# Kernel tuning notes

Measured on AMD Instinct MI355X. Metric: run time of the kernel, lower is better.

## Reference

```python
import jax, jax.numpy as jnp
import numpy as np

B, S, E, H = 2, 2048, 1024, 16
D = E // H


def setup_inputs() -> dict:
    key = jax.random.key(0)
    ks = jax.random.split(key, 8)
    hidden_states = jax.random.normal(ks[0], (B, S, E), dtype=jnp.float32)
    # q/k/v projections: small random init
    Wq = jax.random.normal(ks[1], (E, E), dtype=jnp.float32) * 0.02
    Wk = jax.random.normal(ks[2], (E, E), dtype=jnp.float32) * 0.02
    Wv = jax.random.normal(ks[3], (E, E), dtype=jnp.float32) * 0.02
    bq = jnp.zeros((E,), jnp.float32)
    bk = jnp.zeros((E,), jnp.float32)
    bv = jnp.zeros((E,), jnp.float32)
    # hedgehog feature maps: identity init (per init_weights_) + small noise
    eye = jnp.eye(E, dtype=jnp.float32)
    Wfq = eye + jax.random.normal(ks[4], (E, E), dtype=jnp.float32) * 0.02
    Wfk = eye + jax.random.normal(ks[5], (E, E), dtype=jnp.float32) * 0.02
    bfq = jnp.zeros((E,), jnp.float32)
    bfk = jnp.zeros((E,), jnp.float32)
    return dict(hidden_states=hidden_states, Wq=Wq, bq=bq, Wk=Wk, bk=bk,
                Wv=Wv, bv=bv, Wfq=Wfq, bfq=bfq, Wfk=Wfk, bfk=bfk)


def reference(hidden_states, Wq, bq, Wk, bk, Wv, bv, Wfq, bfq, Wfk, bfk):
    b, s, e = hidden_states.shape
    d = e // H
    # feature maps: linear -> linear -> softmax over full hidden dim (before head split)
    q = jax.nn.softmax((hidden_states @ Wq.T + bq) @ Wfq.T + bfq, axis=-1)
    k = jax.nn.softmax((hidden_states @ Wk.T + bk) @ Wfk.T + bfk, axis=-1)
    v = hidden_states @ Wv.T + bv
    split = lambda t: t.reshape(b, s, H, d).transpose(0, 2, 1, 3)  # [B,H,S,D]
    q, k, v = split(q), split(k), split(v)
    scores = jnp.einsum('bhsd,bhtd->bhst', q, k)          # [B,H,S,S], nonnegative
    probs = scores / jnp.sum(scores, axis=-1, keepdims=True)  # sum-normalization
    ctx = jnp.einsum('bhst,bhtd->bhsd', probs, v)
    return ctx.transpose(0, 2, 1, 3).reshape(b, s, e)
```

## Files before the change

### kernel.cpp

```cpp
#include <hip/hip_runtime.h>
#include <math.h>

constexpr int B = 2, S = 2048, E = 1024, H = 16, D = 64;
constexpr int M = B * S;
constexpr int CH = 16;

typedef __attribute__((ext_vector_type(8))) _Float16 half8;
typedef __attribute__((ext_vector_type(4))) float f32x4;
#define MFMA_F16 __builtin_amdgcn_mfma_f32_16x16x32_f16
#define WAITCNT_VM(N) __builtin_amdgcn_s_waitcnt(0xF70 | (N))

__device__ __forceinline__ short f2h(float f) {
  _Float16 h = (_Float16)f;
  short s;
  __builtin_memcpy(&s, &h, 2);
  return s;
}
__device__ __forceinline__ float h2f(short s) {
  _Float16 h;
  __builtin_memcpy(&h, &s, 2);
  return (float)h;
}

__device__ __forceinline__ void gload16(const void* g, const void* l) {
  __builtin_amdgcn_global_load_lds(
      (const __attribute__((address_space(1))) unsigned*)g,
      (__attribute__((address_space(3))) unsigned*)l, 16, 0, 0);
}

struct HArgs {
  const short* A;
  const short* Bm;
  const float* bias;
  short* C;
  float* Zrow;
  int doExp;
};

template <int BM, int WEMIT>
__global__ __launch_bounds__(256, 3) void gemmh(HArgs g0, HArgs g1, HArgs g2, int K, int N) {
  const HArgs h = (blockIdx.z == 0) ? g0 : (blockIdx.z == 1 ? g1 : g2);
  constexpr int SA = BM / 16;
  constexpr int TOT = SA + 8;
  constexpr int PW = TOT / 4;
  constexpr int MT = BM / 32;
  __shared__ short lds[2][TOT * 512];

  const int tid = threadIdx.x, wave = tid >> 6, lane = tid & 63;
  const int bm = blockIdx.x * BM, bn = blockIdx.y * 128;

  const short* gb[PW];
#pragma unroll
  for (int j = 0; j < PW; ++j) {
    const int n = wave * PW + j;
    const short* src; int seg, rowbase;
    if (n < SA) { src = h.A;  seg = n;      rowbase = bm; }
    else        { src = h.Bm; seg = n - SA; rowbase = bn; }
    const int r = seg * 16 + (lane >> 2);
    const int p = lane & 3;
    const int q = (p - ((r >> 1) & 3)) & 3;
    gb[j] = src + (size_t)(rowbase + r) * K + q * 8;
  }

  const int fr = lane & 15, fq = lane >> 4;
  const int wm = (wave & 1) * (BM / 2), wn = (wave >> 1) * 64;
  int ao[MT], bo[4];
#pragma unroll
  for (int mi = 0; mi < MT; ++mi) {
    const int r = wm + mi * 16 + fr;
    ao[mi] = r * 32 + (((fq + ((r >> 1) & 3)) & 3)) * 8;
  }
#pragma unroll
  for (int ni = 0; ni < 4; ++ni) {
    const int r = wn + ni * 16 + fr;
    bo[ni] = BM * 32 + r * 32 + (((fq + ((r >> 1) & 3)) & 3)) * 8;
  }

  f32x4 acc[MT][4] = {};
  const int ldsW = wave * PW * 512;

  auto stageAll = [&](int buf, int k0) {
#pragma unroll
    for (int j = 0; j < PW; ++j)
      gload16(gb[j] + k0, &lds[buf][ldsW + j * 512]);
  };

  stageAll(0, 0);
  stageAll(1, 32);
  int buf = 0;
  for (int k0 = 0; k0 < K; k0 += 32) {
    if (k0 + 32 < K) WAITCNT_VM(PW); else WAITCNT_VM(0);
    __builtin_amdgcn_s_barrier();
    half8 ah[MT], bh4[4];
#pragma unroll
    for (int mi = 0; mi < MT; ++mi) ah[mi] = *(const half8*)&lds[buf][ao[mi]];
#pragma unroll
    for (int ni = 0; ni < 4; ++ni) bh4[ni] = *(const half8*)&lds[buf][bo[ni]];
#pragma unroll
    for (int mi = 0; mi < MT; ++mi)
#pragma unroll
      for (int ni = 0; ni < 4; ++ni)
        acc[mi][ni] = MFMA_F16(ah[mi], bh4[ni], acc[mi][ni], 0, 0, 0);
    __builtin_amdgcn_s_barrier();
    if (k0 + 64 < K) stageAll(buf, k0 + 64);
    buf ^= 1;
  }

  if (WEMIT == 0) {
    short* C = h.C;
    float bv4[4];
#pragma unroll
    for (int ni = 0; ni < 4; ++ni) bv4[ni] = h.bias[bn + wn + ni * 16 + fr];
#pragma unroll
    for (int mi = 0; mi < MT; ++mi)
#pragma unroll
      for (int r2 = 0; r2 < 4; ++r2) {
        const int m = bm + wm + mi * 16 + fq * 4 + r2;
        float vals[4];
#pragma unroll
        for (int ni = 0; ni < 4; ++ni) vals[ni] = acc[mi][ni][r2] + bv4[ni];
        if (h.doExp) {
#pragma unroll
          for (int ni = 0; ni < 4; ++ni) vals[ni] = __expf(vals[ni]);
        }
        if (h.Zrow) {
          float es = vals[0] + vals[1] + vals[2] + vals[3];
#pragma unroll
          for (int off = 1; off < 16; off <<= 1) es += __shfl_xor(es, off, 16);
          if (fr == 0) atomicAdd(&h.Zrow[m], es);
        }
#pragma unroll
        for (int ni = 0; ni < 4; ++ni)
          C[(size_t)m * N + bn + wn + ni * 16 + fr] = f2h(vals[ni]);
      }
  } else {
    short* C = h.C;
#pragma unroll
    for (int ni = 0; ni < 4; ++ni) {
      const int n = bn + wn + ni * 16 + fr;
#pragma unroll
      for (int mi = 0; mi < MT; ++mi) {
        const int m0 = bm + wm + mi * 16 + fq * 4;
#pragma unroll
        for (int r2 = 0; r2 < 4; ++r2)
          C[(size_t)(m0 + r2) * N + n] = f2h(acc[mi][ni][r2]);
      }
    }
  }
}

__global__ __launch_bounds__(256) void prep(
    const float* __restrict__ hs, short* hs_f,
    const float* __restrict__ Wfq, short* Wfq_f,
    const float* __restrict__ Wfk, short* Wfk_f,
    const float* __restrict__ Wv, short* Wv_f,
    const float* __restrict__ Wq, short* WqT_f,
    const float* __restrict__ Wk, short* WkT_f,
    const float* __restrict__ bq, const float* __restrict__ bfq, float* bcQ,
    const float* __restrict__ bk, const float* __restrict__ bfk, float* bcK,
    float* Zk) {
  __shared__ float tb[32][33];
  const int blk = blockIdx.x, tid = threadIdx.x;
  if (blk < 1024) {
#pragma unroll
    for (int p = 0; p < 4; ++p) {
      const int i = blk * 1024 + p * 256 + tid;
      float4 v = ((const float4*)hs)[i];
      ((short4*)hs_f)[i] = make_short4(f2h(v.x), f2h(v.y), f2h(v.z), f2h(v.w));
    }
  } else if (blk < 1792) {
    const int base = blk - 1024;
    const float* src = (base < 256) ? Wfq : (base < 512 ? Wfk : Wv);
    short* dst = (base < 256) ? Wfq_f : (base < 512 ? Wfk_f : Wv_f);
    const int bb = base & 255;
#pragma unroll
    for (int p = 0; p < 4; ++p) {
      const int i = bb * 1024 + p * 256 + tid;
      float4 v = ((const float4*)src)[i];
      ((short4*)dst)[i] = make_short4(f2h(v.x), f2h(v.y), f2h(v.z), f2h(v.w));
    }
  } else if (blk < 3840) {
    const int t = blk - 1792;
    const float* in = (t < 1024) ? Wq : Wk;
    short* oh = (t < 1024) ? WqT_f : WkT_f;
    const int tt = t & 1023;
    const int bx = (tt & 31) * 32, by = (tt >> 5) * 32;
    const int x = tid & 31, y0 = tid >> 5;
#pragma unroll
    for (int i = 0; i < 32; i += 8) tb[y0 + i][x] = in[(size_t)(by + y0 + i) * E + bx + x];
    __syncthreads();
#pragma unroll
    for (int i = 0; i < 32; i += 8)
      oh[(size_t)(bx + y0 + i) * E + by + x] = f2h(tb[x][y0 + i]);
  } else if (blk < 4352) {
    const int t = blk - 3840;
    const float* Wf = (t < 256) ? Wfq : Wfk;
    const float* bin = (t < 256) ? bq : bk;
    const float* bf = (t < 256) ? bfq : bfk;
    float* o = (t < 256) ? bcQ : bcK;
    const int n = (t & 255) * 4 + (tid >> 6);
    const int lane = tid & 63;
    float sacc = 0.f;
    for (int j = lane; j < E; j += 64) sacc += Wf[(size_t)n * E + j] * bin[j];
#pragma unroll
    for (int off = 32; off; off >>= 1) sacc += __shfl_xor(sacc, off, 64);
    if (lane == 0) o[n] = sacc + bf[n];
  } else {
#pragma unroll
    for (int p = 0; p < 4; ++p)
      ((float4*)Zk)[p * 256 + tid] = make_float4(0.f, 0.f, 0.f, 0.f);
  }
}

__global__ __launch_bounds__(256) void kv_part(const short* __restrict__ kh,
                                               const short* __restrict__ vh,
                                               const float* __restrict__ Zk,
                                               float* __restrict__ KVp,
                                               float* __restrict__ ksump) {
  const int bh = blockIdx.x;
  const int b = bh / H, h = bh % H;
  const int t0 = blockIdx.y * 128;
  const short* kbase = kh + (size_t)b * S * E + (size_t)h * D;
  const short* vbase = vh + (size_t)b * S * E + (size_t)h * D;
  __shared__ float ks[16][D];
  __shared__ float vs[16][D];
  __shared__ float invZs[128];
  const int tid = threadIdx.x;
  if (tid < 128) invZs[tid] = 1.0f / Zk[b * S + t0 + tid];
  const int a4 = tid & 15, b4 = tid >> 4;
  const int lt = tid >> 4, d4 = (tid & 15) * 4;
  float acc[4][4] = {};
  float ksm[4] = {};
  for (int ts = 0; ts < 128; ts += 16) {
    __syncthreads();
    const size_t roff = (size_t)(t0 + ts + lt) * E + d4;
    short4 k4 = *(const short4*)(kbase + roff);
    short4 v4 = *(const short4*)(vbase + roff);
    const float iz = invZs[ts + lt];
    ks[lt][d4 + 0] = h2f(k4.x) * iz; ks[lt][d4 + 1] = h2f(k4.y) * iz;
    ks[lt][d4 + 2] = h2f(k4.z) * iz; ks[lt][d4 + 3] = h2f(k4.w) * iz;
    vs[lt][d4 + 0] = h2f(v4.x); vs[lt][d4 + 1] = h2f(v4.y);
    vs[lt][d4 + 2] = h2f(v4.z); vs[lt][d4 + 3] = h2f(v4.w);
    __syncthreads();
#pragma unroll
    for (int tt = 0; tt < 16; ++tt) {
      float kk4[4], vv4[4];
#pragma unroll
      for (int i = 0; i < 4; ++i) kk4[i] = ks[tt][a4 * 4 + i];
#pragma unroll
      for (int j = 0; j < 4; ++j) vv4[j] = vs[tt][b4 * 4 + j];
#pragma unroll
      for (int i = 0; i < 4; ++i) {
        ksm[i] += kk4[i];
#pragma unroll
        for (int j = 0; j < 4; ++j) acc[i][j] = fmaf(kk4[i], vv4[j], acc[i][j]);
      }
    }
  }
  float* kvout = KVp + ((size_t)bh * CH + blockIdx.y) * 4096;
#pragma unroll
  for (int i = 0; i < 4; ++i)
    *(float4*)&kvout[(a4 * 4 + i) * 64 + b4 * 4] =
        make_float4(acc[i][0], acc[i][1], acc[i][2], acc[i][3]);
  if (b4 == 0)
    *(float4*)&ksump[((size_t)bh * CH + blockIdx.y) * 64 + a4 * 4] =
        make_float4(ksm[0], ksm[1], ksm[2], ksm[3]);
}

__global__ __launch_bounds__(256) void kv_reduce(const float* __restrict__ KVp,
                                                 const float* __restrict__ ksump,
                                                 float* __restrict__ KV,
                                                 float* __restrict__ ksum) {
  const int bh = blockIdx.x, tid = threadIdx.x;
  for (int i = tid; i < 1024; i += 256) {
    float4 s = make_float4(0.f, 0.f, 0.f, 0.f);
#pragma unroll
    for (int c = 0; c < CH; ++c) {
      float4 p = ((const float4*)(KVp + ((size_t)bh * CH + c) * 4096))[i];
      s.x += p.x; s.y += p.y; s.z += p.z; s.w += p.w;
    }
    ((float4*)(KV + (size_t)bh * 4096))[i] = s;
  }
  if (tid < 16) {
    float4 s = make_float4(0.f, 0.f, 0.f, 0.f);
#pragma unroll
    for (int c = 0; c < CH; ++c) {
      float4 p = ((const float4*)(ksump + ((size_t)bh * CH + c) * 64))[tid];
      s.x += p.x; s.y += p.y; s.z += p.z; s.w += p.w;
    }
    ((float4*)(ksum + bh * 64))[tid] = s;
  }
}

__global__ __launch_bounds__(256) void out_v7(const short* __restrict__ uh,
                                              const float* __restrict__ KV,
                                              const float* __restrict__ ksum,
                                              float* __restrict__ out) {
  const int bh = blockIdx.x;
  const int b = bh >> 4, h = bh & 15;
  __shared__ float KVs[64][64];
  __shared__ float kss[64];
  __shared__ float qs[4][4][64];
  const int tid = threadIdx.x, wave = tid >> 6, lane = tid & 63;
  const int r2 = lane >> 4, g = lane & 15;
  for (int i = tid; i < 1024; i += 256)
    ((float4*)KVs)[i] = ((const float4*)(KV + (size_t)bh * 4096))[i];
  if (tid < 64) kss[tid] = ksum[bh * 64 + tid];
  __syncthreads();
  const float4 ks4 = *(const float4*)&kss[g * 4];
  const int row0 = blockIdx.y * 64 + wave * 16;
#pragma unroll
  for (int it = 0; it < 4; ++it) {
    const int row = row0 + it * 4 + r2;
    const size_t rowoff = ((size_t)b * S + row) * E + h * 64;
    short4 us = *(const short4*)(uh + rowoff + g * 4);
    float4 u = make_float4(h2f(us.x), h2f(us.y), h2f(us.z), h2f(us.w));
    float dn = u.x * ks4.x + u.y * ks4.y + u.z * ks4.z + u.w * ks4.w;
#pragma unroll
    for (int off = 1; off < 16; off <<= 1) dn += __shfl_xor(dn, off, 16);
    *(float4*)&qs[wave][r2][g * 4] = u;
    __syncthreads();
    float nx = 0.f, ny = 0.f, nz = 0.f, nw = 0.f;
#pragma unroll
    for (int d = 0; d < 64; ++d) {
      const float qd = qs[wave][r2][d];
      const float4 kv = *(const float4*)&KVs[d][g * 4];
      nx = fmaf(qd, kv.x, nx); ny = fmaf(qd, kv.y, ny);
      nz = fmaf(qd, kv.z, nz); nw = fmaf(qd, kv.w, nw);
    }
    const float inv = 1.0f / dn;
    float4 o4 = make_float4(nx * inv, ny * inv, nz * inv, nw * inv);
    *(float4*)(out + rowoff + g * 4) = o4;
    __syncthreads();
  }
}

extern "C" void kernel_launch(void* const* d_in, const int* in_sizes, int n_in,
                              void* d_out, int out_size, void* d_ws, size_t ws_size,
                              hipStream_t stream) {
  const float* hs = (const float*)d_in[0];
  const float* Wq = (const float*)d_in[1];
  const float* bq = (const float*)d_in[2];
  const float* Wk = (const float*)d_in[3];
  const float* bk = (const float*)d_in[4];
  const float* Wv = (const float*)d_in[5];
  const float* bv = (const float*)d_in[6];
  const float* Wfq = (const float*)d_in[7];
  const float* bfq = (const float*)d_in[8];
  const float* Wfk = (const float*)d_in[9];
  const float* bfk = (const float*)d_in[10];
  float* out = (float*)d_out;

  const size_t MEG = 1024 * 1024;
  float* ws = (float*)d_ws;
  short* uh = (short*)ws;
  short* kh = (short*)(ws + 2 * MEG);
  short* vh = (short*)(ws + 4 * MEG);
  short* hs_f = (short*)(ws + 6 * MEG);
  short* Wfq_f = (short*)(ws + 8 * MEG);
  short* Wfk_f = (short*)(ws + 8 * MEG + 512 * 1024);
  short* Wv_f = (short*)(ws + 9 * MEG);
  short* WqT_f = (short*)(ws + 9 * MEG + 512 * 1024);
  short* WkT_f = (short*)(ws + 10 * MEG);
  short* WcQ_f = (short*)(ws + 10 * MEG + 512 * 1024);
  short* WcK_f = (short*)(ws + 11 * MEG);
  float* bcQ = ws + 12 * MEG;
  float* bcK = bcQ + 1024;
  float* Zk = bcK + 1024;
  float* KV = Zk + M;
  float* ksum = KV + 32 * 4096;
  float* KVp = (float*)hs_f;
  float* ksump = (float*)Wfq_f;

  prep<<<4353, 256, 0, stream>>>(hs, hs_f, Wfq, Wfq_f, Wfk, Wfk_f, Wv, Wv_f,
                                 Wq, WqT_f, Wk, WkT_f,
                                 bq, bfq, bcQ, bk, bfk, bcK, Zk);
  HArgs w0 = {Wfq_f, WqT_f, nullptr, WcQ_f, nullptr, 0};
  HArgs w1 = {Wfk_f, WkT_f, nullptr, WcK_f, nullptr, 0};
  gemmh<64, 1><<<dim3(16, 8, 2), 256, 0, stream>>>(w0, w1, w1, E, E);
  HArgs gq = {hs_f, WcQ_f, bcQ, uh, nullptr, 1};
  HArgs gk = {hs_f, WcK_f, bcK, kh, Zk, 1};
  HArgs gv = {hs_f, Wv_f, bv, vh, nullptr, 0};
  gemmh<128, 0><<<dim3(32, 8, 3), 256, 0, stream>>>(gq, gk, gv, E, E);
  kv_part<<<dim3(B * H, CH), 256, 0, stream>>>(kh, vh, Zk, KVp, ksump);
  kv_reduce<<<B * H, 256, 0, stream>>>(KVp, ksump, KV, ksum);
  out_v7<<<dim3(B * H, S / 64), 256, 0, stream>>>(uh, KV, ksum, out);
}
```

Measured before the change: 189.0 us.

## Concatenate QKV weights into one wide GEMM and fold KV reduce into output kernel

```diff
diff --git a/kernel.cpp b/kernel.cpp
--- a/kernel.cpp
+++ b/kernel.cpp
@@ -3,7 +3,8 @@
 
 constexpr int B = 2, S = 2048, E = 1024, H = 16, D = 64;
 constexpr int M = B * S;
-constexpr int CH = 16;
+constexpr int NBIG = 3072;
+constexpr int CH = 8;
 
 typedef __attribute__((ext_vector_type(8))) _Float16 half8;
 typedef __attribute__((ext_vector_type(4))) float f32x4;
@@ -28,40 +29,26 @@
       (__attribute__((address_space(3))) unsigned*)l, 16, 0, 0);
 }
 
-struct HArgs {
-  const short* A;
-  const short* Bm;
-  const float* bias;
-  short* C;
-  float* Zrow;
-  int doExp;
-};
-
-template <int BM, int WEMIT>
-__global__ __launch_bounds__(256, 3) void gemmh(HArgs g0, HArgs g1, HArgs g2, int K, int N) {
-  const HArgs h = (blockIdx.z == 0) ? g0 : (blockIdx.z == 1 ? g1 : g2);
-  constexpr int SA = BM / 16;
-  constexpr int TOT = SA + 8;
-  constexpr int PW = TOT / 4;
-  constexpr int MT = BM / 32;
-  __shared__ short lds[2][TOT * 512];
-
+template <int BM>
+__device__ __forceinline__ void gemm_core(const short* __restrict__ A,
+                                          const short* __restrict__ Bm,
+                                          int bm, int bn, int K, short* lds,
+                                          f32x4 (&acc)[BM / 32][4]) {
+  constexpr int SA = BM / 16, TOT = SA + 8, PW = TOT / 4, MT = BM / 32;
   const int tid = threadIdx.x, wave = tid >> 6, lane = tid & 63;
-  const int bm = blockIdx.x * BM, bn = blockIdx.y * 128;
 
   const short* gb[PW];
 #pragma unroll
   for (int j = 0; j < PW; ++j) {
     const int n = wave * PW + j;
     const short* src; int seg, rowbase;
-    if (n < SA) { src = h.A;  seg = n;      rowbase = bm; }
-    else        { src = h.Bm; seg = n - SA; rowbase = bn; }
+    if (n < SA) { src = A;  seg = n;      rowbase = bm; }
+    else        { src = Bm; seg = n - SA; rowbase = bn; }
     const int r = seg * 16 + (lane >> 2);
     const int p = lane & 3;
     const int q = (p - ((r >> 1) & 3)) & 3;
     gb[j] = src + (size_t)(rowbase + r) * K + q * 8;
   }
-
   const int fr = lane & 15, fq = lane >> 4;
   const int wm = (wave & 1) * (BM / 2), wn = (wave >> 1) * 64;
   int ao[MT], bo[4];
@@ -75,16 +62,12 @@
     const int r = wn + ni * 16 + fr;
     bo[ni] = BM * 32 + r * 32 + (((fq + ((r >> 1) & 3)) & 3)) * 8;
   }
-
-  f32x4 acc[MT][4] = {};
   const int ldsW = wave * PW * 512;
-
   auto stageAll = [&](int buf, int k0) {
 #pragma unroll
     for (int j = 0; j < PW; ++j)
-      gload16(gb[j] + k0, &lds[buf][ldsW + j * 512]);
+      gload16(gb[j] + k0, &lds[buf * TOT * 512 + ldsW + j * 512]);
   };
-
   stageAll(0, 0);
   stageAll(1, 32);
   int buf = 0;
@@ -92,10 +75,11 @@
     if (k0 + 32 < K) WAITCNT_VM(PW); else WAITCNT_VM(0);
     __builtin_amdgcn_s_barrier();
     half8 ah[MT], bh4[4];
-#pragma unroll
-    for (int mi = 0; mi < MT; ++mi) ah[mi] = *(const half8*)&lds[buf][ao[mi]];
-#pragma unroll
-    for (int ni = 0; ni < 4; ++ni) bh4[ni] = *(const half8*)&lds[buf][bo[ni]];
+    const int bb = buf * TOT * 512;
+#pragma unroll
+    for (int mi = 0; mi < MT; ++mi) ah[mi] = *(const half8*)&lds[bb + ao[mi]];
+#pragma unroll
+    for (int ni = 0; ni < 4; ++ni) bh4[ni] = *(const half8*)&lds[bb + bo[ni]];
 #pragma unroll
     for (int mi = 0; mi < MT; ++mi)
 #pragma unroll
@@ -105,71 +89,21 @@
     if (k0 + 64 < K) stageAll(buf, k0 + 64);
     buf ^= 1;
   }
-
-  if (WEMIT == 0) {
-    short* C = h.C;
-    float bv4[4];
-#pragma unroll
-    for (int ni = 0; ni < 4; ++ni) bv4[ni] = h.bias[bn + wn + ni * 16 + fr];
-#pragma unroll
-    for (int mi = 0; mi < MT; ++mi)
-#pragma unroll
-      for (int r2 = 0; r2 < 4; ++r2) {
-        const int m = bm + wm + mi * 16 + fq * 4 + r2;
-        float vals[4];
-#pragma unroll
-        for (int ni = 0; ni < 4; ++ni) vals[ni] = acc[mi][ni][r2] + bv4[ni];
-        if (h.doExp) {
-#pragma unroll
-          for (int ni = 0; ni < 4; ++ni) vals[ni] = __expf(vals[ni]);
-        }
-        if (h.Zrow) {
-          float es = vals[0] + vals[1] + vals[2] + vals[3];
-#pragma unroll
-          for (int off = 1; off < 16; off <<= 1) es += __shfl_xor(es, off, 16);
-          if (fr == 0) atomicAdd(&h.Zrow[m], es);
-        }
-#pragma unroll
-        for (int ni = 0; ni < 4; ++ni)
-          C[(size_t)m * N + bn + wn + ni * 16 + fr] = f2h(vals[ni]);
-      }
-  } else {
-    short* C = h.C;
-#pragma unroll
-    for (int ni = 0; ni < 4; ++ni) {
-      const int n = bn + wn + ni * 16 + fr;
-#pragma unroll
-      for (int mi = 0; mi < MT; ++mi) {
-        const int m0 = bm + wm + mi * 16 + fq * 4;
-#pragma unroll
-        for (int r2 = 0; r2 < 4; ++r2)
-          C[(size_t)(m0 + r2) * N + n] = f2h(acc[mi][ni][r2]);
-      }
-    }
-  }
-}
-
-__global__ __launch_bounds__(256) void prep(
-    const float* __restrict__ hs, short* hs_f,
+}
+
+__global__ __launch_bounds__(256) void prep_w(
     const float* __restrict__ Wfq, short* Wfq_f,
     const float* __restrict__ Wfk, short* Wfk_f,
     const float* __restrict__ Wv, short* Wv_f,
     const float* __restrict__ Wq, short* WqT_f,
     const float* __restrict__ Wk, short* WkT_f,
-    const float* __restrict__ bq, const float* __restrict__ bfq, float* bcQ,
-    const float* __restrict__ bk, const float* __restrict__ bfk, float* bcK,
-    float* Zk) {
+    const float* __restrict__ bq, const float* __restrict__ bfq,
+    const float* __restrict__ bk, const float* __restrict__ bfk,
+    const float* __restrict__ bv, float* bcat, float* Zk) {
   __shared__ float tb[32][33];
   const int blk = blockIdx.x, tid = threadIdx.x;
-  if (blk < 1024) {
-#pragma unroll
-    for (int p = 0; p < 4; ++p) {
-      const int i = blk * 1024 + p * 256 + tid;
-      float4 v = ((const float4*)hs)[i];
-      ((short4*)hs_f)[i] = make_short4(f2h(v.x), f2h(v.y), f2h(v.z), f2h(v.w));
-    }
-  } else if (blk < 1792) {
-    const int base = blk - 1024;
+  if (blk < 768) {
+    const int base = blk;
     const float* src = (base < 256) ? Wfq : (base < 512 ? Wfk : Wv);
     short* dst = (base < 256) ? Wfq_f : (base < 512 ? Wfk_f : Wv_f);
     const int bb = base & 255;
@@ -179,8 +113,8 @@
       float4 v = ((const float4*)src)[i];
       ((short4*)dst)[i] = make_short4(f2h(v.x), f2h(v.y), f2h(v.z), f2h(v.w));
     }
-  } else if (blk < 3840) {
-    const int t = blk - 1792;
+  } else if (blk < 2816) {
+    const int t = blk - 768;
     const float* in = (t < 1024) ? Wq : Wk;
     short* oh = (t < 1024) ? WqT_f : WkT_f;
     const int tt = t & 1023;
@@ -192,12 +126,12 @@
 #pragma unroll
     for (int i = 0; i < 32; i += 8)
       oh[(size_t)(bx + y0 + i) * E + by + x] = f2h(tb[x][y0 + i]);
-  } else if (blk < 4352) {
-    const int t = blk - 3840;
+  } else if (blk < 3328) {
+    const int t = blk - 2816;
     const float* Wf = (t < 256) ? Wfq : Wfk;
     const float* bin = (t < 256) ? bq : bk;
     const float* bf = (t < 256) ? bfq : bfk;
-    float* o = (t < 256) ? bcQ : bcK;
+    float* o = (t < 256) ? bcat : bcat + 1024;
     const int n = (t & 255) * 4 + (tid >> 6);
     const int lane = tid & 63;
     float sacc = 0.f;
@@ -206,34 +140,111 @@
     for (int off = 32; off; off >>= 1) sacc += __shfl_xor(sacc, off, 64);
     if (lane == 0) o[n] = sacc + bf[n];
   } else {
+    ((float4*)(bcat + 2048))[tid] = ((const float4*)bv)[tid];
 #pragma unroll
     for (int p = 0; p < 4; ++p)
       ((float4*)Zk)[p * 256 + tid] = make_float4(0.f, 0.f, 0.f, 0.f);
   }
 }
 
-__global__ __launch_bounds__(256) void kv_part(const short* __restrict__ kh,
-                                               const short* __restrict__ vh,
+__global__ __launch_bounds__(256, 3) void wgemm_hs(
+    const short* __restrict__ Wfq_f, const short* __restrict__ WqT_f,
+    const short* __restrict__ Wfk_f, const short* __restrict__ WkT_f,
+    short* __restrict__ Wcat,
+    const float* __restrict__ hs, short* __restrict__ hs_f) {
+  __shared__ short lds[2 * 12 * 512];
+  if (blockIdx.z == 2) {
+    const int bid = blockIdx.y * 16 + blockIdx.x;
+    const int stride = 128 * 256;
+    for (int i = bid * 256 + threadIdx.x; i < M * E / 4; i += stride) {
+      float4 v = ((const float4*)hs)[i];
+      ((short4*)hs_f)[i] = make_short4(f2h(v.x), f2h(v.y), f2h(v.z), f2h(v.w));
+    }
+    return;
+  }
+  const short* A = blockIdx.z ? Wfk_f : Wfq_f;
+  const short* Bm = blockIdx.z ? WkT_f : WqT_f;
+  short* C = Wcat + (size_t)blockIdx.z * E * E;
+  const int bm = blockIdx.x * 64, bn = blockIdx.y * 128;
+  f32x4 acc[2][4] = {};
+  gemm_core<64>(A, Bm, bm, bn, E, lds, acc);
+  const int lane = threadIdx.x & 63, wave = threadIdx.x >> 6;
+  const int fr = lane & 15, fq = lane >> 4;
+  const int wm = (wave & 1) * 32, wn = (wave >> 1) * 64;
+#pragma unroll
+  for (int ni = 0; ni < 4; ++ni) {
+    const int n = bn + wn + ni * 16 + fr;
+#pragma unroll
+    for (int mi = 0; mi < 2; ++mi) {
+      const int m0 = bm + wm + mi * 16 + fq * 4;
+#pragma unroll
+      for (int r2 = 0; r2 < 4; ++r2)
+        C[(size_t)(m0 + r2) * E + n] = f2h(acc[mi][ni][r2]);
+    }
+  }
+}
+
+__global__ __launch_bounds__(256, 3) void gemm_big(
+    const short* __restrict__ hs_f, const short* __restrict__ Wcat,
+    const float* __restrict__ bcat, short* __restrict__ Cb,
+    float* __restrict__ Zk) {
+  __shared__ short lds[2 * 16 * 512];
+  const int bm = blockIdx.y * 128, bn = blockIdx.x * 128;
+  f32x4 acc[4][4] = {};
+  gemm_core<128>(hs_f, Wcat, bm, bn, E, lds, acc);
+  const int lane = threadIdx.x & 63, wave = threadIdx.x >> 6;
+  const int fr = lane & 15, fq = lane >> 4;
+  const int wm = (wave & 1) * 64, wn = (wave >> 1) * 64;
+  const bool doExp = (bn < 2048);
+  const bool doZ = (bn >= 1024) && (bn < 2048);
+  float bv4[4];
+#pragma unroll
+  for (int ni = 0; ni < 4; ++ni) bv4[ni] = bcat[bn + wn + ni * 16 + fr];
+#pragma unroll
+  for (int mi = 0; mi < 4; ++mi)
+#pragma unroll
+    for (int r2 = 0; r2 < 4; ++r2) {
+      const int m = bm + wm + mi * 16 + fq * 4 + r2;
+      float vals[4];
+#pragma unroll
+      for (int ni = 0; ni < 4; ++ni) vals[ni] = acc[mi][ni][r2] + bv4[ni];
+      if (doExp) {
+#pragma unroll
+        for (int ni = 0; ni < 4; ++ni) vals[ni] = __expf(vals[ni]);
+      }
+      if (doZ) {
+        float es = vals[0] + vals[1] + vals[2] + vals[3];
+#pragma unroll
+        for (int off = 1; off < 16; off <<= 1) es += __shfl_xor(es, off, 16);
+        if (fr == 0) atomicAdd(&Zk[m], es);
+      }
+#pragma unroll
+      for (int ni = 0; ni < 4; ++ni)
+        Cb[(size_t)m * NBIG + bn + wn + ni * 16 + fr] = f2h(vals[ni]);
+    }
+}
+
+__global__ __launch_bounds__(256) void kv_part(const short* __restrict__ Cb,
                                                const float* __restrict__ Zk,
                                                float* __restrict__ KVp,
                                                float* __restrict__ ksump) {
   const int bh = blockIdx.x;
   const int b = bh / H, h = bh % H;
-  const int t0 = blockIdx.y * 128;
-  const short* kbase = kh + (size_t)b * S * E + (size_t)h * D;
-  const short* vbase = vh + (size_t)b * S * E + (size_t)h * D;
+  const int t0 = blockIdx.y * 256;
+  const short* kbase = Cb + (size_t)b * S * NBIG + 1024 + h * D;
+  const short* vbase = Cb + (size_t)b * S * NBIG + 2048 + h * D;
   __shared__ float ks[16][D];
   __shared__ float vs[16][D];
-  __shared__ float invZs[128];
+  __shared__ float invZs[256];
   const int tid = threadIdx.x;
-  if (tid < 128) invZs[tid] = 1.0f / Zk[b * S + t0 + tid];
+  invZs[tid] = 1.0f / Zk[b * S + t0 + tid];
   const int a4 = tid & 15, b4 = tid >> 4;
   const int lt = tid >> 4, d4 = (tid & 15) * 4;
   float acc[4][4] = {};
   float ksm[4] = {};
-  for (int ts = 0; ts < 128; ts += 16) {
-    __syncthreads();
-    const size_t roff = (size_t)(t0 + ts + lt) * E + d4;
+  for (int ts = 0; ts < 256; ts += 16) {
+    __syncthreads();
+    const size_t roff = (size_t)(t0 + ts + lt) * NBIG + d4;
     short4 k4 = *(const short4*)(kbase + roff);
     short4 v4 = *(const short4*)(vbase + roff);
     const float iz = invZs[ts + lt];
@@ -267,34 +278,9 @@
         make_float4(ksm[0], ksm[1], ksm[2], ksm[3]);
 }
 
-__global__ __launch_bounds__(256) void kv_reduce(const float* __restrict__ KVp,
-                                                 const float* __restrict__ ksump,
-                                                 float* __restrict__ KV,
-                                                 float* __restrict__ ksum) {
-  const int bh = blockIdx.x, tid = threadIdx.x;
-  for (int i = tid; i < 1024; i += 256) {
-    float4 s = make_float4(0.f, 0.f, 0.f, 0.f);
-#pragma unroll
-    for (int c = 0; c < CH; ++c) {
-      float4 p = ((const float4*)(KVp + ((size_t)bh * CH + c) * 4096))[i];
-      s.x += p.x; s.y += p.y; s.z += p.z; s.w += p.w;
-    }
-    ((float4*)(KV + (size_t)bh * 4096))[i] = s;
-  }
-  if (tid < 16) {
-    float4 s = make_float4(0.f, 0.f, 0.f, 0.f);
-#pragma unroll
-    for (int c = 0; c < CH; ++c) {
-      float4 p = ((const float4*)(ksump + ((size_t)bh * CH + c) * 64))[tid];
-      s.x += p.x; s.y += p.y; s.z += p.z; s.w += p.w;
-    }
-    ((float4*)(ksum + bh * 64))[tid] = s;
-  }
-}
-
-__global__ __launch_bounds__(256) void out_v7(const short* __restrict__ uh,
-                                              const float* __restrict__ KV,
-                                              const float* __restrict__ ksum,
+__global__ __launch_bounds__(256) void out_v8(const short* __restrict__ Cb,
+                                              const float* __restrict__ KVp,
+                                              const float* __restrict__ ksump,
                                               float* __restrict__ out) {
   const int bh = blockIdx.x;
   const int b = bh >> 4, h = bh & 15;
@@ -303,17 +289,31 @@
   __shared__ float qs[4][4][64];
   const int tid = threadIdx.x, wave = tid >> 6, lane = tid & 63;
   const int r2 = lane >> 4, g = lane & 15;
-  for (int i = tid; i < 1024; i += 256)
-    ((float4*)KVs)[i] = ((const float4*)(KV + (size_t)bh * 4096))[i];
-  if (tid < 64) kss[tid] = ksum[bh * 64 + tid];
+  for (int i = tid; i < 1024; i += 256) {
+    float4 s = make_float4(0.f, 0.f, 0.f, 0.f);
+#pragma unroll
+    for (int c = 0; c < CH; ++c) {
+      float4 p = ((const float4*)(KVp + ((size_t)bh * CH + c) * 4096))[i];
+      s.x += p.x; s.y += p.y; s.z += p.z; s.w += p.w;
+    }
+    ((float4*)KVs)[i] = s;
+  }
+  if (tid < 16) {
+    float4 s = make_float4(0.f, 0.f, 0.f, 0.f);
+#pragma unroll
+    for (int c = 0; c < CH; ++c) {
+      float4 p = ((const float4*)(ksump + ((size_t)bh * CH + c) * 64))[tid];
+      s.x += p.x; s.y += p.y; s.z += p.z; s.w += p.w;
+    }
+    ((float4*)kss)[tid] = s;
+  }
   __syncthreads();
   const float4 ks4 = *(const float4*)&kss[g * 4];
   const int row0 = blockIdx.y * 64 + wave * 16;
 #pragma unroll
   for (int it = 0; it < 4; ++it) {
     const int row = row0 + it * 4 + r2;
-    const size_t rowoff = ((size_t)b * S + row) * E + h * 64;
-    short4 us = *(const short4*)(uh + rowoff + g * 4);
+    short4 us = *(const short4*)(Cb + (size_t)(b * S + row) * NBIG + h * 64 + g * 4);
     float4 u = make_float4(h2f(us.x), h2f(us.y), h2f(us.z), h2f(us.w));
     float dn = u.x * ks4.x + u.y * ks4.y + u.z * ks4.z + u.w * ks4.w;
 #pragma unroll
@@ -330,7 +330,8 @@
     }
     const float inv = 1.0f / dn;
     float4 o4 = make_float4(nx * inv, ny * inv, nz * inv, nw * inv);
-    *(float4*)(out + rowoff + g * 4) = o4;
+    const size_t rowoff = ((size_t)b * S + row) * E + h * 64 + g * 4;
+    *(float4*)(out + rowoff) = o4;
     __syncthreads();
   }
 }
@@ -353,36 +354,25 @@
 
   const size_t MEG = 1024 * 1024;
   float* ws = (float*)d_ws;
-  short* uh = (short*)ws;
-  short* kh = (short*)(ws + 2 * MEG);
-  short* vh = (short*)(ws + 4 * MEG);
-  short* hs_f = (short*)(ws + 6 * MEG);
-  short* Wfq_f = (short*)(ws + 8 * MEG);
-  short* Wfk_f = (short*)(ws + 8 * MEG + 512 * 1024);
-  short* Wv_f = (short*)(ws + 9 * MEG);
-  short* WqT_f = (short*)(ws + 9 * MEG + 512 * 1024);
-  short* WkT_f = (short*)(ws + 10 * MEG);
-  short* WcQ_f = (short*)(ws + 10 * MEG + 512 * 1024);
-  short* WcK_f = (short*)(ws + 11 * MEG);
-  float* bcQ = ws + 12 * MEG;
-  float* bcK = bcQ + 1024;
-  float* Zk = bcK + 1024;
-  float* KV = Zk + M;
-  float* ksum = KV + 32 * 4096;
-  float* KVp = (float*)hs_f;
-  float* ksump = (float*)Wfq_f;
-
-  prep<<<4353, 256, 0, stream>>>(hs, hs_f, Wfq, Wfq_f, Wfk, Wfk_f, Wv, Wv_f,
-                                 Wq, WqT_f, Wk, WkT_f,
-                                 bq, bfq, bcQ, bk, bfk, bcK, Zk);
-  HArgs w0 = {Wfq_f, WqT_f, nullptr, WcQ_f, nullptr, 0};
-  HArgs w1 = {Wfk_f, WkT_f, nullptr, WcK_f, nullptr, 0};
-  gemmh<64, 1><<<dim3(16, 8, 2), 256, 0, stream>>>(w0, w1, w1, E, E);
-  HArgs gq = {hs_f, WcQ_f, bcQ, uh, nullptr, 1};
-  HArgs gk = {hs_f, WcK_f, bcK, kh, Zk, 1};
-  HArgs gv = {hs_f, Wv_f, bv, vh, nullptr, 0};
-  gemmh<128, 0><<<dim3(32, 8, 3), 256, 0, stream>>>(gq, gk, gv, E, E);
-  kv_part<<<dim3(B * H, CH), 256, 0, stream>>>(kh, vh, Zk, KVp, ksump);
-  kv_reduce<<<B * H, 256, 0, stream>>>(KVp, ksump, KV, ksum);
-  out_v7<<<dim3(B * H, S / 64), 256, 0, stream>>>(uh, KV, ksum, out);
-}
+  short* hs_f = (short*)ws;
+  short* Wfq_f = (short*)(ws + 2 * MEG);
+  short* Wfk_f = (short*)(ws + 2 * MEG + MEG / 2);
+  short* WqT_f = (short*)(ws + 3 * MEG);
+  short* WkT_f = (short*)(ws + 3 * MEG + MEG / 2);
+  short* Wcat = (short*)(ws + 4 * MEG);
+  short* Wv_f = Wcat + 2 * MEG;
+  float* bcat = ws + 6 * MEG;
+  float* Zk = bcat + 4096;
+  float* KVp = ws + 7 * MEG;
+  float* ksump = ws + 8 * MEG;
+  short* Cbig = (short*)(ws + 9 * MEG);
+
+  prep_w<<<3329, 256, 0, stream>>>(Wfq, Wfq_f, Wfk, Wfk_f, Wv, Wv_f,
+                                   Wq, WqT_f, Wk, WkT_f,
+                                   bq, bfq, bk, bfk, bv, bcat, Zk);
+  wgemm_hs<<<dim3(16, 8, 3), 256, 0, stream>>>(Wfq_f, WqT_f, Wfk_f, WkT_f,
+                                               Wcat, hs, hs_f);
+  gemm_big<<<dim3(24, 32), 256, 0, stream>>>(hs_f, Wcat, bcat, Cbig, Zk);
+  kv_part<<<dim3(B * H, CH), 256, 0, stream>>>(Cbig, Zk, KVp, ksump);
+  out_v8<<<dim3(B * H, S / 64), 256, 0, stream>>>(Cbig, KVp, ksump, out);
+}
```

New measurement: 182.5 us. 3.4% less time.
